# Kernel tuning notes

Hardware: AMD Instinct MI355X
Metric: run time of the kernel (lower is better)

The kernel has to match this reference:

```python
import jax, jax.numpy as jnp
import numpy as np

EPS = 1e-9
LN_EPS = 1e-5

def _ln(t, g, b):
    m = t.mean(-1, keepdims=True)
    v = ((t - m) ** 2).mean(-1, keepdims=True)
    return (t - m) / jnp.sqrt(v + LN_EPS) * g + b

def _dwconv(t, w, b):
    # t: (B,S,H), w: (H,1,4) depthwise. torch pads 3 on both sides then slices [:S],
    # which equals causal left-pad of 3.
    y = jax.lax.conv_general_dilated(
        t.transpose(0, 2, 1), w, window_strides=(1,), padding=[(3, 0)],
        feature_group_count=w.shape[0], dimension_numbers=("NCH", "OIH", "NCH"))
    return y.transpose(0, 2, 1) + b

def _forward(x, Wq, Wk, Wv, Wo, Wg, We1, We2, Wd1, Wd2, Wa1, Wa2,
             conv_w, conv_b, qn_g, qn_b, kn_g, kn_b, mW1, mb1, mW2, mb2, chunk_size):
    B, S, D = x.shape
    H = Wk.shape[1]
    M = mW1.shape[0]
    q = x @ Wq; k = x @ Wk; v = x @ Wv
    eta = jax.nn.softplus((x @ We1) @ We2)
    delta = jax.nn.softplus((x @ Wd1) @ Wd2)
    alpha = jax.nn.sigmoid((x @ Wa1) @ Wa2)
    q = _ln(_dwconv(q, conv_w, conv_b), qn_g, qn_b)  # computed but unused downstream, as in source
    k = _ln(_dwconv(k, conv_w, conv_b), kn_g, kn_b)
    v = _dwconv(v, conv_w, conv_b)
    n = S // chunk_size
    chunk = lambda t: t.reshape(B, n, chunk_size, H).transpose(1, 0, 2, 3)  # (n,B,C,H)
    xs = (chunk(k), chunk(v), chunk(eta), chunk(delta), chunk(alpha))
    state0 = (jnp.broadcast_to(mW1, (B, M, H)), jnp.broadcast_to(mb1, (B, M)),
              jnp.broadcast_to(mW2, (B, H, M)), jnp.broadcast_to(mb2, (B, H)))

    def step(state, inp):
        W1, b1, W2, b2 = state
        kc, vc, ec, dc, ac = inp  # each (B,C,H)
        inter = jnp.einsum("bch,bmh->bcm", kc, W1) + b1[:, None, :]
        act = jax.nn.gelu(inter, approximate=False)
        out = jnp.einsum("bcm,bhm->bch", act, W2) + b2[:, None, :]
        err = out - vc
        en = jnp.sqrt(jnp.sum(err * err, axis=-1, keepdims=True))  # (B,C,1)
        grad = jnp.where(en > dc, dc * err / (en + EPS), err)
        aw = ac[:, -1, :].mean(-1)[:, None, None]
        ew = ec[:, -1, :].mean(-1)[:, None, None]
        us = grad.mean(1, keepdims=True)   # (B,1,H)
        am = act.mean(1, keepdims=True)    # (B,1,M)
        W1g = jnp.einsum("bom,boh->bmh", am, us)
        W2g = jnp.einsum("boh,bom->bhm", us, am)
        nW1 = aw * W1 - ew * W1g
        nW2 = aw * W2 - ew * W2g
        ab = ac[:, -1, :]; eb = ec[:, -1, :]
        b2u = grad.mean(1)
        b1u = jnp.einsum("bch,bhm->bcm", grad, nW2).mean(1)
        nb2 = ab * b2 - eb * b2u
        nb1 = ab.mean(-1, keepdims=True) * b1 - eb.mean(-1, keepdims=True) * b1u
        # torch updates state under no_grad -> detach
        new_state = jax.tree_util.tree_map(jax.lax.stop_gradient, (nW1, nb1, nW2, nb2))
        return new_state, out

    _, outs = jax.lax.scan(step, state0, xs)  # (n,B,C,H)
    combined = outs.transpose(1, 0, 2, 3).reshape(B, S, H)
    return (combined @ Wo) * jax.nn.sigmoid(x @ Wg)

def setup_inputs():
    key = jax.random.key(0)
    B, S, D, H, M, R = 4, 4096, 1024, 128, 256, 64
    ks = jax.random.split(key, 23)
    g = lambda i, shp, s: jax.random.normal(ks[i], shp, jnp.float32) * s
    return {
        "x": g(0, (B, S, D), 1.0),
        "Wq": g(1, (D, H), 0.02), "Wk": g(2, (D, H), 0.02), "Wv": g(3, (D, H), 0.02),
        "Wo": g(4, (H, D), 0.02), "Wg": g(5, (D, D), 0.02),
        "We1": g(6, (D, R), 0.02), "We2": g(7, (R, H), 0.02),
        "Wd1": g(8, (D, R), 0.02), "Wd2": g(9, (R, H), 0.02),
        "Wa1": g(10, (D, R), 0.02), "Wa2": g(11, (R, H), 0.02),
        "conv_w": g(12, (H, 1, 4), 0.2), "conv_b": g(13, (H,), 0.02),
        "qn_g": jnp.ones((H,), jnp.float32), "qn_b": jnp.zeros((H,), jnp.float32),
        "kn_g": jnp.ones((H,), jnp.float32), "kn_b": jnp.zeros((H,), jnp.float32),
        "mW1": g(14, (M, H), 0.05), "mb1": g(15, (M,), 0.02),
        "mW2": g(16, (H, M), 0.05), "mb2": g(17, (H,), 0.02),
        "chunk_size": 64,
    }

def reference(x, Wq, Wk, Wv, Wo, Wg, We1, We2, Wd1, Wd2, Wa1, Wa2,
              conv_w, conv_b, qn_g, qn_b, kn_g, kn_b, mW1, mb1, mW2, mb2, chunk_size):
    return _forward(x, Wq, Wk, Wv, Wo, Wg, We1, We2, Wd1, Wd2, Wa1, Wa2,
                    conv_w, conv_b, qn_g, qn_b, kn_g, kn_b, mW1, mb1, mW2, mb2, chunk_size)
```

## Files before the change

kernel.cpp:

```cpp
#include <hip/hip_runtime.h>
#include <math.h>

#define Bq 4
#define Sq 4096
#define Dq 1024
#define Hq 128
#define Mq 256
#define Rq 64
#define Cq 64
#define NCHUNK 64
#define BSq (Bq*Sq)

typedef __attribute__((ext_vector_type(8))) short short8;
typedef __attribute__((ext_vector_type(4))) float f32x4;

__device__ __forceinline__ float softplusf_(float x){
  return fmaxf(x,0.f) + log1pf(expf(-fabsf(x)));
}
__device__ __forceinline__ float sigmoidf_(float x){
  return 1.f/(1.f+__expf(-x));
}
__device__ __forceinline__ unsigned short bf16rn(float x){
  unsigned u = __float_as_uint(x);
  u += 0x7fffu + ((u>>16)&1u);
  return (unsigned short)(u>>16);
}
__device__ __forceinline__ float bf16tof(unsigned short s){
  return __uint_as_float(((unsigned)s)<<16);
}
__device__ __forceinline__ unsigned cvt_pk_bf16(float a, float b){
  unsigned r;
  asm("v_cvt_pk_bf16_f32 %0, %1, %2" : "=v"(r) : "v"(a), "v"(b));
  return r;
}
__device__ __forceinline__ float lo16f(unsigned p){ return __uint_as_float(p<<16); }
__device__ __forceinline__ float hi16f(unsigned p){ return __uint_as_float(p & 0xffff0000u); }
union pk8 { unsigned u[4]; short8 s; };

__device__ __forceinline__ float gelu_fast(float x){
  float z  = x*0.70710678118f;
  float az = fabsf(z);
  float t  = __builtin_amdgcn_rcpf(fmaf(0.3275911f, az, 1.f));
  float p  = fmaf(t, 1.061405429f, -1.453152027f);
  p = fmaf(t, p, 1.421413741f);
  p = fmaf(t, p, -0.284496736f);
  p = fmaf(t, p, 0.254829592f);
  p = p*t;
  float e  = __expf(-az*az);
  float er = copysignf(1.f - p*e, z);
  return 0.5f*x*(1.f + er);
}

template<int BN, int ACT>
__global__ __launch_bounds__(256) void gemm_bf3(
    const float* __restrict__ Af,
    const unsigned short* __restrict__ BhT, const unsigned short* __restrict__ BlT,
    float* __restrict__ C, const float* __restrict__ gate, int N, int K)
{
  constexpr int BM = 128;
  constexpr int PK = 40;
  constexpr int TN = BN/32;
  __shared__ __align__(16) unsigned short As[2][BM*PK];
  __shared__ __align__(16) unsigned short Bs[2][BN*PK];
  const int tid = threadIdx.x;
  const int bm = blockIdx.y*BM, bn = blockIdx.x*BN;
  const int wv = tid>>6, lane = tid&63;
  const int n16 = lane&15, q = lane>>4;
  const int wm = wv>>1, wn = wv&1;

  f32x4 acc[4][TN];
  #pragma unroll
  for (int i=0;i<4;i++){
    #pragma unroll
    for (int j=0;j<TN;j++){ f32x4 z={0.f,0.f,0.f,0.f}; acc[i][j]=z; }
  }
  for (int k0=0;k0<K;k0+=32){
    #pragma unroll
    for (int c0=0;c0<BM*8;c0+=256){
      int c = c0 + tid;
      int row = c>>3, kg = (c&7)*4;
      float4 v = *(const float4*)&Af[(size_t)(bm+row)*K + k0+kg];
      unsigned hp0 = cvt_pk_bf16(v.x, v.y), hp1 = cvt_pk_bf16(v.z, v.w);
      unsigned lp0 = cvt_pk_bf16(v.x-lo16f(hp0), v.y-hi16f(hp0));
      unsigned lp1 = cvt_pk_bf16(v.z-lo16f(hp1), v.w-hi16f(hp1));
      int off = row*PK+kg;
      *(unsigned*)&As[0][off]   = hp0;
      *(unsigned*)&As[0][off+2] = hp1;
      *(unsigned*)&As[1][off]   = lp0;
      *(unsigned*)&As[1][off+2] = lp1;
    }
    #pragma unroll
    for (int c0=0;c0<BN*4;c0+=256){
      int c = c0 + tid;
      int row = c>>2, kg = (c&3)*8;
      *(short8*)&Bs[0][row*PK+kg] = *(const short8*)&BhT[(size_t)(bn+row)*K + k0+kg];
      *(short8*)&Bs[1][row*PK+kg] = *(const short8*)&BlT[(size_t)(bn+row)*K + k0+kg];
    }
    __syncthreads();
    short8 a_h[4], a_l[4], b_h[TN], b_l[TN];
    #pragma unroll
    for (int i=0;i<4;i++){
      int r = wm*64 + i*16 + n16;
      a_h[i] = *(const short8*)&As[0][r*PK + q*8];
      a_l[i] = *(const short8*)&As[1][r*PK + q*8];
    }
    #pragma unroll
    for (int j=0;j<TN;j++){
      int r = wn*(BN/2) + j*16 + n16;
      b_h[j] = *(const short8*)&Bs[0][r*PK + q*8];
      b_l[j] = *(const short8*)&Bs[1][r*PK + q*8];
    }
    #pragma unroll
    for (int i=0;i<4;i++){
      #pragma unroll
      for (int j=0;j<TN;j++){
        acc[i][j] = __builtin_amdgcn_mfma_f32_16x16x32_bf16(a_h[i], b_h[j], acc[i][j], 0,0,0);
        acc[i][j] = __builtin_amdgcn_mfma_f32_16x16x32_bf16(a_l[i], b_h[j], acc[i][j], 0,0,0);
        acc[i][j] = __builtin_amdgcn_mfma_f32_16x16x32_bf16(a_h[i], b_l[j], acc[i][j], 0,0,0);
      }
    }
    __syncthreads();
  }
  #pragma unroll
  for (int i=0;i<4;i++){
    #pragma unroll
    for (int j=0;j<TN;j++){
      #pragma unroll
      for (int r=0;r<4;r++){
        int row = bm + wm*64 + i*16 + q*4 + r;
        int col = bn + wn*(BN/2) + j*16 + n16;
        float v = acc[i][j][r];
        if (ACT==1) v = softplusf_(v);
        else if (ACT==2) v = sigmoidf_(v);
        else if (ACT==3) v *= sigmoidf_(gate[(size_t)row*N+col]);
        C[(size_t)row*N+col] = v;
      }
    }
  }
}

template<int BN>
__global__ __launch_bounds__(256) void gemm_bb(
    const unsigned short* __restrict__ Ah, const unsigned short* __restrict__ Al,
    const unsigned short* __restrict__ BhT, const unsigned short* __restrict__ BlT,
    float* __restrict__ C0, float* __restrict__ C1, float* __restrict__ C2, int K)
{
  constexpr int BM = 128;
  constexpr int PK = 40;
  constexpr int TN = BN/32;
  __shared__ __align__(16) unsigned short As[2][BM*PK];
  __shared__ __align__(16) unsigned short Bs[2][BN*PK];
  const int tid = threadIdx.x;
  const int bx = blockIdx.x;
  const int bm = blockIdx.y*BM;
  const int bnB = bx*BN;
  float* __restrict__ C = (bx==0) ? C0 : ((bx==1) ? C1 : C2);
  const int wv = tid>>6, lane = tid&63;
  const int n16 = lane&15, q = lane>>4;
  const int wm = wv>>1, wn = wv&1;

  f32x4 acc[4][TN];
  #pragma unroll
  for (int i=0;i<4;i++){
    #pragma unroll
    for (int j=0;j<TN;j++){ f32x4 z={0.f,0.f,0.f,0.f}; acc[i][j]=z; }
  }
  for (int k0=0;k0<K;k0+=32){
    #pragma unroll
    for (int c0=0;c0<BM*4;c0+=256){
      int c = c0 + tid;
      int row = c>>2, kg = (c&3)*8;
      *(short8*)&As[0][row*PK+kg] = *(const short8*)&Ah[(size_t)(bm+row)*K + k0+kg];
      *(short8*)&As[1][row*PK+kg] = *(const short8*)&Al[(size_t)(bm+row)*K + k0+kg];
    }
    #pragma unroll
    for (int c0=0;c0<BN*4;c0+=256){
      int c = c0 + tid;
      int row = c>>2, kg = (c&3)*8;
      *(short8*)&Bs[0][row*PK+kg] = *(const short8*)&BhT[(size_t)(bnB+row)*K + k0+kg];
      *(short8*)&Bs[1][row*PK+kg] = *(const short8*)&BlT[(size_t)(bnB+row)*K + k0+kg];
    }
    __syncthreads();
    short8 a_h[4], a_l[4], b_h[TN], b_l[TN];
    #pragma unroll
    for (int i=0;i<4;i++){
      int r = wm*64 + i*16 + n16;
      a_h[i] = *(const short8*)&As[0][r*PK + q*8];
      a_l[i] = *(const short8*)&As[1][r*PK + q*8];
    }
    #pragma unroll
    for (int j=0;j<TN;j++){
      int r = wn*(BN/2) + j*16 + n16;
      b_h[j] = *(const short8*)&Bs[0][r*PK + q*8];
      b_l[j] = *(const short8*)&Bs[1][r*PK + q*8];
    }
    #pragma unroll
    for (int i=0;i<4;i++){
      #pragma unroll
      for (int j=0;j<TN;j++){
        acc[i][j] = __builtin_amdgcn_mfma_f32_16x16x32_bf16(a_h[i], b_h[j], acc[i][j], 0,0,0);
        acc[i][j] = __builtin_amdgcn_mfma_f32_16x16x32_bf16(a_l[i], b_h[j], acc[i][j], 0,0,0);
        acc[i][j] = __builtin_amdgcn_mfma_f32_16x16x32_bf16(a_h[i], b_l[j], acc[i][j], 0,0,0);
      }
    }
    __syncthreads();
  }
  #pragma unroll
  for (int i=0;i<4;i++){
    #pragma unroll
    for (int j=0;j<TN;j++){
      #pragma unroll
      for (int r=0;r<4;r++){
        int row = bm + wm*64 + i*16 + q*4 + r;
        int col = wn*(BN/2) + j*16 + n16;
        C[(size_t)row*BN+col] = acc[i][j][r];
      }
    }
  }
}

__global__ void splitT(const float* __restrict__ W,
                       unsigned short* __restrict__ hT, unsigned short* __restrict__ lT,
                       int K, int N)
{
  int idx = blockIdx.x*256 + threadIdx.x;
  if (idx >= N*K) return;
  int nn = idx / K, k = idx - nn*K;
  float v = W[(size_t)k*N + nn];
  unsigned short h = bf16rn(v);
  hT[idx] = h;
  lT[idx] = bf16rn(v - bf16tof(h));
}

__global__ __launch_bounds__(256) void splitX(const float* __restrict__ A,
    unsigned short* __restrict__ h, unsigned short* __restrict__ l)
{
  size_t idx = ((size_t)blockIdx.x*256 + threadIdx.x)*4;
  float4 v = *(const float4*)&A[idx];
  unsigned hp0 = cvt_pk_bf16(v.x, v.y), hp1 = cvt_pk_bf16(v.z, v.w);
  unsigned lp0 = cvt_pk_bf16(v.x-lo16f(hp0), v.y-hi16f(hp0));
  unsigned lp1 = cvt_pk_bf16(v.z-lo16f(hp1), v.w-hi16f(hp1));
  *(unsigned*)&h[idx]   = hp0;
  *(unsigned*)&h[idx+2] = hp1;
  *(unsigned*)&l[idx]   = lp0;
  *(unsigned*)&l[idx+2] = lp1;
}

__global__ __launch_bounds__(128) void conv_ln_kernel(
  const float* __restrict__ k_raw, const float* __restrict__ v_raw,
  const float* __restrict__ conv_w, const float* __restrict__ conv_b,
  const float* __restrict__ kn_g, const float* __restrict__ kn_b,
  float* __restrict__ k_out, float* __restrict__ v_out)
{
  int s = blockIdx.x, b = blockIdx.y, which = blockIdx.z;
  int h = threadIdx.x;
  const float* src = (which==0) ? k_raw : v_raw;
  float acc = conv_b[h];
  #pragma unroll
  for (int j=0;j<4;j++){
    int ss = s-3+j;
    if (ss>=0) acc += conv_w[h*4+j]*src[((size_t)b*Sq+ss)*Hq + h];
  }
  if (which==0){
    __shared__ float red[4];
    float sv = acc, s2 = acc*acc;
    #pragma unroll
    for (int off=32; off>0; off>>=1){
      sv += __shfl_down(sv, off, 64);
      s2 += __shfl_down(s2, off, 64);
    }
    if ((h&63)==0){ red[(h>>6)*2]=sv; red[(h>>6)*2+1]=s2; }
    __syncthreads();
    float mean = (red[0]+red[2])*(1.f/128.f);
    float var  = (red[1]+red[3])*(1.f/128.f) - mean*mean;
    float y = (acc-mean)*rsqrtf(var+1e-5f)*kn_g[h]+kn_b[h];
    k_out[((size_t)b*Sq+s)*Hq + h] = y;
  } else {
    v_out[((size_t)b*Sq+s)*Hq + h] = acc;
  }
}

#define OFF_KCH   0
#define OFF_KCL   16384
#define OFF_ACTH  32768
#define OFF_SAM   65536
#define OFF_SUS   66560
#define OFF_PEN   67072
#define OFF_DRED  70144
#define OFF_SUU   78336
#define OFF_SAB   78368
#define OFF_SEB   78880
#define OFF_SABP  79392
#define OFF_SEBP  79400
#define LDS_TOTAL 79408

__global__ __launch_bounds__(512, 2) void fused_scan_wg(
  const float* __restrict__ k_ln, const float* __restrict__ v_c,
  const float* __restrict__ eta, const float* __restrict__ delta,
  const float* __restrict__ alpha,
  const float* __restrict__ mW1, const float* __restrict__ mb1,
  const float* __restrict__ mW2, const float* __restrict__ mb2,
  float* __restrict__ combined,
  const float* __restrict__ x,
  const unsigned short* __restrict__ WgTh, const unsigned short* __restrict__ WgTl,
  float* __restrict__ glog)
{
  __shared__ __align__(16) char smem[LDS_TOTAL];
  const int blk = blockIdx.x;
  const int tid = threadIdx.x;
  const int wv = tid >> 6;
  const int lane = tid & 63;
  const int n = lane & 15;
  const int q = lane >> 4;

  if (blk >= 4){
    unsigned short* As_h = (unsigned short*)smem;
    unsigned short* As_l = As_h + 128*40;
    unsigned short* Bs_h = As_l + 128*40;
    unsigned short* Bs_l = Bs_h + 128*40;
    const int g = blk - 4;
    const int bm = (g>>3)*128, bn = (g&7)*128;
    const int wm = wv&3, wn = wv>>2;
    f32x4 acc[2][4];
    #pragma unroll
    for (int i=0;i<2;i++){
      #pragma unroll
      for (int j=0;j<4;j++){ f32x4 z={0.f,0.f,0.f,0.f}; acc[i][j]=z; }
    }
    for (int k0=0;k0<Dq;k0+=32){
      #pragma unroll
      for (int r=0;r<2;r++){
        int idx = tid + 512*r;
        int row = idx>>3, kg = (idx&7)*4;
        float4 v = *(const float4*)&x[(size_t)(bm+row)*Dq + k0+kg];
        unsigned hp0 = cvt_pk_bf16(v.x, v.y), hp1 = cvt_pk_bf16(v.z, v.w);
        unsigned lp0 = cvt_pk_bf16(v.x-lo16f(hp0), v.y-hi16f(hp0));
        unsigned lp1 = cvt_pk_bf16(v.z-lo16f(hp1), v.w-hi16f(hp1));
        int off = row*40+kg;
        *(unsigned*)&As_h[off]   = hp0;
        *(unsigned*)&As_h[off+2] = hp1;
        *(unsigned*)&As_l[off]   = lp0;
        *(unsigned*)&As_l[off+2] = lp1;
      }
      {
        int row = tid>>2, kg = (tid&3)*8;
        *(short8*)&Bs_h[row*40+kg] = *(const short8*)&WgTh[(size_t)(bn+row)*Dq + k0+kg];
        *(short8*)&Bs_l[row*40+kg] = *(const short8*)&WgTl[(size_t)(bn+row)*Dq + k0+kg];
      }
      __syncthreads();
      short8 a_h[2], a_l[2], b_h[4], b_l[4];
      #pragma unroll
      for (int i=0;i<2;i++){
        int r = wm*32 + i*16 + n;
        a_h[i] = *(const short8*)&As_h[r*40 + q*8];
        a_l[i] = *(const short8*)&As_l[r*40 + q*8];
      }
      #pragma unroll
      for (int j=0;j<4;j++){
        int r = wn*64 + j*16 + n;
        b_h[j] = *(const short8*)&Bs_h[r*40 + q*8];
        b_l[j] = *(const short8*)&Bs_l[r*40 + q*8];
      }
      #pragma unroll
      for (int i=0;i<2;i++){
        #pragma unroll
        for (int j=0;j<4;j++){
          acc[i][j] = __builtin_amdgcn_mfma_f32_16x16x32_bf16(a_h[i], b_h[j], acc[i][j], 0,0,0);
          acc[i][j] = __builtin_amdgcn_mfma_f32_16x16x32_bf16(a_l[i], b_h[j], acc[i][j], 0,0,0);
          acc[i][j] = __builtin_amdgcn_mfma_f32_16x16x32_bf16(a_h[i], b_l[j], acc[i][j], 0,0,0);
        }
      }
      __syncthreads();
    }
    #pragma unroll
    for (int i=0;i<2;i++){
      #pragma unroll
      for (int j=0;j<4;j++){
        #pragma unroll
        for (int r=0;r<4;r++){
          int row = bm + wm*32 + i*16 + q*4 + r;
          int col = bn + wn*64 + j*16 + n;
          glog[(size_t)row*Dq+col] = acc[i][j][r];
        }
      }
    }
    return;
  }

  unsigned short* kc_hi  = (unsigned short*)(smem + OFF_KCH);
  unsigned short* kc_lo  = (unsigned short*)(smem + OFF_KCL);
  unsigned short* act_hi = (unsigned short*)(smem + OFF_ACTH);
  float* Sam = (float*)(smem + OFF_SAM);
  float* Sus = (float*)(smem + OFF_SUS);
  float* pen = (float*)(smem + OFF_PEN);
  float* Dred= (float*)(smem + OFF_DRED);
  float* Suu = (float*)(smem + OFF_SUU);
  float* Sab = (float*)(smem + OFF_SAB);
  float* Seb = (float*)(smem + OFF_SEB);
  float* Sabp = (float*)(smem + OFF_SABP);
  float* Sebp = (float*)(smem + OFF_SEBP);

  const int b = blk;
  const int h = wv*16 + n;
  float w1m[2][4][8];
  float w2m[8][8];
  float b1reg[2];
  float b2n[4];
  #pragma unroll
  for (int tt=0;tt<2;tt++){
    int m = (2*wv+tt)*16 + n;
    #pragma unroll
    for (int ks=0;ks<4;ks++){
      const float* p = mW1 + (size_t)m*Hq + ks*32 + q*8;
      #pragma unroll
      for (int j=0;j<8;j++) w1m[tt][ks][j] = p[j];
    }
    b1reg[tt] = mb1[m];
  }
  {
    #pragma unroll
    for (int ks2=0;ks2<8;ks2++){
      const float* p = mW2 + (size_t)h*Mq + ks2*32 + q*8;
      #pragma unroll
      for (int j=0;j<8;j++) w2m[ks2][j] = p[j];
    }
    #pragma unroll
    for (int r=0;r<4;r++) b2n[r] = mb2[wv*16 + q*4 + r];
  }
  float aw = 0.f, ew = 0.f;
  float am_own[2] = {0.f, 0.f};

  float4 pf[4];
  {
    const size_t base0 = (size_t)b*Sq*Hq;
    #pragma unroll
    for (int r4=0;r4<4;r4++){
      int i4 = tid + 512*r4;
      pf[r4] = *(const float4*)(k_ln + base0 + (size_t)i4*4);
    }
  }

  for (int t=0; t<NCHUNK; ++t){
    const size_t base = ((size_t)b*Sq + (size_t)t*Cq)*Hq;
    #pragma unroll
    for (int r4=0;r4<4;r4++){
      int i4 = tid + 512*r4;
      int c = i4>>5, h0 = (i4&31)<<2;
      float4 v = pf[r4];
      int pg  = (h0>>3) ^ (c & 15);
      int off = c*Hq + (pg<<3) + (h0&7);
      unsigned hp0 = cvt_pk_bf16(v.x, v.y), hp1 = cvt_pk_bf16(v.z, v.w);
      unsigned lp0 = cvt_pk_bf16(v.x-lo16f(hp0), v.y-hi16f(hp0));
      unsigned lp1 = cvt_pk_bf16(v.z-lo16f(hp1), v.w-hi16f(hp1));
      *(unsigned*)&kc_hi[off]   = hp0;
      *(unsigned*)&kc_hi[off+2] = hp1;
      *(unsigned*)&kc_lo[off]   = lp0;
      *(unsigned*)&kc_lo[off+2] = lp1;
    }
    float ab_=0.f, eb_=0.f;
    if (tid < 128){
      ab_ = alpha[base + 63*Hq + tid];
      eb_ = eta[base + 63*Hq + tid];
    }
    __syncthreads();

    if (t > 0){
      float4 s0[4], s1[4];
      #pragma unroll
      for (int ks=0;ks<4;ks++){
        s0[ks] = *(const float4*)&Sus[ks*32 + q*8];
        s1[ks] = *(const float4*)&Sus[ks*32 + q*8 + 4];
      }
      float4 u0 = *(const float4*)&Suu[0];
      float4 u1 = *(const float4*)&Suu[4];
      float uu = u0.x+u0.y+u0.z+u0.w+u1.x+u1.y+u1.z+u1.w;
      #pragma unroll
      for (int tt=0;tt<2;tt++){
        int m = (2*wv+tt)*16 + n;
        float amm = am_own[tt];
        float eam = ew*amm;
        #pragma unroll
        for (int ks=0;ks<4;ks++){
          #pragma unroll
          for (int j=0;j<4;j++){
            w1m[tt][ks][j]   = aw*w1m[tt][ks][j]   - eam*s0[ks][j];
            w1m[tt][ks][j+4] = aw*w1m[tt][ks][j+4] - eam*s1[ks][j];
          }
        }
        float dsum = 0.f;
        #pragma unroll
        for (int w8=0;w8<8;w8++) dsum += Dred[w8*256 + m];
        b1reg[tt] = aw*b1reg[tt] - ew*(aw*dsum - ew*uu*amm);
      }
    }

    f32x4 acc1[2][4];
    #pragma unroll
    for (int tt=0;tt<2;tt++){
      #pragma unroll
      for (int ct=0;ct<4;ct++){ f32x4 z={0.f,0.f,0.f,0.f}; acc1[tt][ct]=z; }
    }
    __builtin_amdgcn_s_setprio(1);
    #pragma unroll
    for (int ks=0;ks<4;ks++){
      pk8 BH[2], BL[2];
      #pragma unroll
      for (int tt=0;tt<2;tt++){
        #pragma unroll
        for (int jp=0;jp<4;jp++){
          float a0 = w1m[tt][ks][2*jp], a1 = w1m[tt][ks][2*jp+1];
          unsigned hp = cvt_pk_bf16(a0, a1);
          BH[tt].u[jp] = hp;
          BL[tt].u[jp] = cvt_pk_bf16(a0 - lo16f(hp), a1 - hi16f(hp));
        }
      }
      #pragma unroll
      for (int ct=0;ct<4;ct++){
        int c = ct*16 + n;
        int off = c*Hq + ((((ks*4+q)^n))<<3);
        short8 ah = *(const short8*)&kc_hi[off];
        short8 al = *(const short8*)&kc_lo[off];
        #pragma unroll
        for (int tt=0;tt<2;tt++){
          acc1[tt][ct] = __builtin_amdgcn_mfma_f32_16x16x32_bf16(ah, BH[tt].s, acc1[tt][ct], 0,0,0);
          acc1[tt][ct] = __builtin_amdgcn_mfma_f32_16x16x32_bf16(al, BH[tt].s, acc1[tt][ct], 0,0,0);
          acc1[tt][ct] = __builtin_amdgcn_mfma_f32_16x16x32_bf16(ah, BL[tt].s, acc1[tt][ct], 0,0,0);
        }
      }
    }
    __builtin_amdgcn_s_setprio(0);
    #pragma unroll
    for (int tt=0;tt<2;tt++){
      int m = (2*wv+tt)*16 + n;
      float b1v = b1reg[tt];
      float amsum = 0.f;
      #pragma unroll
      for (int ct=0;ct<4;ct++){
        #pragma unroll
        for (int r=0;r<4;r++){
          float g = gelu_fast(acc1[tt][ct][r] + b1v);
          amsum += g;
          int c = ct*16 + q*4 + r;
          int pg = (m>>3) ^ (c & 15);
          act_hi[c*Mq + (pg<<3) + (m&7)] = bf16rn(g);
        }
      }
      amsum += __shfl_xor(amsum, 16, 64);
      amsum += __shfl_xor(amsum, 32, 64);
      am_own[tt] = amsum*(1.f/64.f);
      if (q==0) Sam[m] = am_own[tt];
    }
    if (tid < 128){ Sab[tid] = ab_; Seb[tid] = eb_; }
    if (wv < 2){
      float a2 = ab_, e2 = eb_;
      #pragma unroll
      for (int mk=1;mk<64;mk<<=1){ a2 += __shfl_xor(a2,mk,64); e2 += __shfl_xor(e2,mk,64); }
      if (lane==0){ Sabp[wv] = a2; Sebp[wv] = e2; }
    }
    __syncthreads();

    float vv[4][4], dd[4][4];
    #pragma unroll
    for (int ct=0;ct<4;ct++){
      #pragma unroll
      for (int r=0;r<4;r++){
        int c = ct*16 + n;
        int h2 = wv*16 + q*4 + r;
        vv[ct][r] = v_c[base + (size_t)c*Hq + h2];
        dd[ct][r] = delta[base + (size_t)c*Hq + h2];
      }
    }

    f32x4 acc2[4];
    #pragma unroll
    for (int ct=0;ct<4;ct++){ f32x4 z={0.f,0.f,0.f,0.f}; acc2[ct]=z; }
    __builtin_amdgcn_s_setprio(1);
    #pragma unroll
    for (int ks2=0;ks2<8;ks2++){
      pk8 BH, BL;
      #pragma unroll
      for (int jp=0;jp<4;jp++){
        float a0 = w2m[ks2][2*jp], a1 = w2m[ks2][2*jp+1];
        unsigned hp = cvt_pk_bf16(a0, a1);
        BH.u[jp] = hp;
        BL.u[jp] = cvt_pk_bf16(a0 - lo16f(hp), a1 - hi16f(hp));
      }
      #pragma unroll
      for (int ct=0;ct<4;ct++){
        int c = ct*16 + n;
        int off = c*Mq + ((((ks2*4+q)^n))<<3);
        short8 ah = *(const short8*)&act_hi[off];
        acc2[ct] = __builtin_amdgcn_mfma_f32_16x16x32_bf16(BH.s, ah, acc2[ct], 0,0,0);
        acc2[ct] = __builtin_amdgcn_mfma_f32_16x16x32_bf16(BL.s, ah, acc2[ct], 0,0,0);
      }
    }
    __builtin_amdgcn_s_setprio(0);

    {
      const size_t basen = ((size_t)b*Sq + (size_t)((t+1<NCHUNK)?(t+1):t)*Cq)*Hq;
      #pragma unroll
      for (int r4=0;r4<4;r4++){
        int i4 = tid + 512*r4;
        pf[r4] = *(const float4*)(k_ln + basen + (size_t)i4*4);
      }
    }

    float err[4][4];
    {
      float* cb = combined + base;
      #pragma unroll
      for (int ct=0;ct<4;ct++){
        #pragma unroll
        for (int r=0;r<4;r++){
          int c = ct*16 + n;
          int h2 = wv*16 + q*4 + r;
          float o = acc2[ct][r] + b2n[r];
          cb[(size_t)c*Hq + h2] = o;
          err[ct][r] = o - vv[ct][r];
        }
      }
      #pragma unroll
      for (int ct=0;ct<4;ct++){
        float s = err[ct][0]*err[ct][0] + err[ct][1]*err[ct][1]
                + err[ct][2]*err[ct][2] + err[ct][3]*err[ct][3];
        s += __shfl_xor(s, 16, 64);
        s += __shfl_xor(s, 32, 64);
        if (q==0) pen[(ct*16+n)*12 + wv] = s;
      }
    }
    __syncthreads();

    aw = (Sabp[0]+Sabp[1])*(1.f/128.f);
    ew = (Sebp[0]+Sebp[1])*(1.f/128.f);

    float en_c[4];
    #pragma unroll
    for (int ct=0;ct<4;ct++){
      int c = ct*16 + n;
      float4 e0 = *(const float4*)&pen[c*12];
      float4 e1 = *(const float4*)&pen[c*12+4];
      en_c[ct] = sqrtf(e0.x+e0.y+e0.z+e0.w+e1.x+e1.y+e1.z+e1.w);
    }
    float us_r[4];
    #pragma unroll
    for (int r=0;r<4;r++){
      float s = 0.f;
      #pragma unroll
      for (int ct=0;ct<4;ct++){
        float e = err[ct][r];
        float dvv = dd[ct][r];
        float en = en_c[ct];
        float g = (en > dvv) ? dvv*e*__builtin_amdgcn_rcpf(en+1e-9f) : e;
        s += g;
      }
      s += __shfl_xor(s,1,64); s += __shfl_xor(s,2,64);
      s += __shfl_xor(s,4,64); s += __shfl_xor(s,8,64);
      us_r[r] = s*(1.f/64.f);
    }
    if (n==0){
      #pragma unroll
      for (int r=0;r<4;r++) Sus[wv*16 + q*4 + r] = us_r[r];
    }
    {
      float uun = us_r[0]*us_r[0] + us_r[1]*us_r[1]
                + us_r[2]*us_r[2] + us_r[3]*us_r[3];
      uun += __shfl_xor(uun, 16, 64);
      uun += __shfl_xor(uun, 32, 64);
      if (lane==0) Suu[wv] = uun;
    }
    #pragma unroll
    for (int r=0;r<4;r++){
      int h2 = wv*16 + q*4 + r;
      b2n[r] = Sab[h2]*b2n[r] - Seb[h2]*us_r[r];
    }
    float ush;
    {
      int src = (n>>2)<<4;
      float p0 = __shfl(us_r[0], src, 64);
      float p1 = __shfl(us_r[1], src, 64);
      float p2 = __shfl(us_r[2], src, 64);
      float p3 = __shfl(us_r[3], src, 64);
      int rr = n&3;
      ush = (rr==0) ? p0 : (rr==1) ? p1 : (rr==2) ? p2 : p3;
    }

    {
      const bool bb0 = (n&1);
      float p1[8][4];
      #pragma unroll
      for (int k2=0;k2<8;k2++){
        #pragma unroll
        for (int l=0;l<4;l++){
          float mine = ush * (bb0 ? w2m[k2][l+4] : w2m[k2][l]);
          float oth  = ush * (bb0 ? w2m[k2][l]   : w2m[k2][l+4]);
          p1[k2][l] = mine + __shfl_xor(oth, 1, 64);
        }
      }
      const bool bb1 = (n>>1)&1;
      float p2[4][4];
      #pragma unroll
      for (int k2=0;k2<4;k2++){
        #pragma unroll
        for (int l=0;l<4;l++){
          float mine = bb1 ? p1[2*k2+1][l] : p1[2*k2][l];
          float oth  = bb1 ? p1[2*k2][l]   : p1[2*k2+1][l];
          p2[k2][l] = mine + __shfl_xor(oth, 2, 64);
        }
      }
      const bool bb2 = (n>>2)&1;
      float p3[2][4];
      #pragma unroll
      for (int k2=0;k2<2;k2++){
        #pragma unroll
        for (int l=0;l<4;l++){
          float mine = bb2 ? p2[2*k2+1][l] : p2[2*k2][l];
          float oth  = bb2 ? p2[2*k2][l]   : p2[2*k2+1][l];
          p3[k2][l] = mine + __shfl_xor(oth, 4, 64);
        }
      }
      const bool bb3 = (n>>3)&1;
      float4 p4;
      {
        float m0 = bb3 ? p3[1][0] : p3[0][0];
        float o0 = bb3 ? p3[0][0] : p3[1][0];
        p4.x = m0 + __shfl_xor(o0, 8, 64);
        float m1 = bb3 ? p3[1][1] : p3[0][1];
        float o1 = bb3 ? p3[0][1] : p3[1][1];
        p4.y = m1 + __shfl_xor(o1, 8, 64);
        float m2 = bb3 ? p3[1][2] : p3[0][2];
        float o2 = bb3 ? p3[0][2] : p3[1][2];
        p4.z = m2 + __shfl_xor(o2, 8, 64);
        float m3 = bb3 ? p3[1][3] : p3[0][3];
        float o3 = bb3 ? p3[0][3] : p3[1][3];
        p4.w = m3 + __shfl_xor(o3, 8, 64);
      }
      int base_m = (n>>1)*32 + q*8 + (n&1)*4;
      *(float4*)&Dred[wv*256 + base_m] = p4;
    }

    {
      float eus = ew*ush;
      #pragma unroll
      for (int ks2=0;ks2<8;ks2++){
        float4 a0 = *(const float4*)&Sam[ks2*32 + q*8];
        float4 a1 = *(const float4*)&Sam[ks2*32 + q*8 + 4];
        #pragma unroll
        for (int j=0;j<4;j++){
          w2m[ks2][j]   = aw*w2m[ks2][j]   - eus*a0[j];
          w2m[ks2][j+4] = aw*w2m[ks2][j+4] - eus*a1[j];
        }
      }
    }
  }
}

extern "C" void kernel_launch(void* const* d_in, const int* in_sizes, int n_in,
                              void* d_out, int out_size, void* d_ws, size_t ws_size,
                              hipStream_t stream)
{
  const float* x    = (const float*)d_in[0];
  const float* Wk   = (const float*)d_in[2];
  const float* Wv   = (const float*)d_in[3];
  const float* Wo   = (const float*)d_in[4];
  const float* Wg   = (const float*)d_in[5];
  const float* We1  = (const float*)d_in[6];
  const float* We2  = (const float*)d_in[7];
  const float* Wd1  = (const float*)d_in[8];
  const float* Wd2  = (const float*)d_in[9];
  const float* Wa1  = (const float*)d_in[10];
  const float* Wa2  = (const float*)d_in[11];
  const float* conv_w = (const float*)d_in[12];
  const float* conv_b = (const float*)d_in[13];
  const float* kn_g = (const float*)d_in[16];
  const float* kn_b = (const float*)d_in[17];
  const float* mW1  = (const float*)d_in[18];
  const float* mb1  = (const float*)d_in[19];
  const float* mW2  = (const float*)d_in[20];
  const float* mb2  = (const float*)d_in[21];
  float* out = (float*)d_out;

  float* ws = (float*)d_ws;
  size_t o = 0;
  float* k_raw = ws + o; o += (size_t)BSq*Hq;
  float* v_raw = ws + o; o += (size_t)BSq*Hq;
  float* te    = ws + o; o += (size_t)BSq*Rq;
  float* td    = ws + o; o += (size_t)BSq*Rq;
  float* ta    = ws + o; o += (size_t)BSq*Rq;
  float* glog  = ws + o; o += (size_t)BSq*Dq;
  float* etab  = ws + o; o += (size_t)BSq*Hq;
  float* deltab= ws + o; o += (size_t)BSq*Hq;
  float* alphab= ws + o; o += (size_t)BSq*Hq;
  float* k_ln  = ws + o; o += (size_t)BSq*Hq;
  float* v_c   = ws + o; o += (size_t)BSq*Hq;
  float* comb  = ws + o; o += (size_t)BSq*Hq;
  unsigned short* us = (unsigned short*)(ws + o);
  size_t u = 0;
  unsigned short *WkvTh = us+u; u += (size_t)2*Hq*Dq;
  unsigned short *WkvTl = us+u; u += (size_t)2*Hq*Dq;
  unsigned short *WedaTh= us+u; u += (size_t)3*Rq*Dq;
  unsigned short *WedaTl= us+u; u += (size_t)3*Rq*Dq;
  unsigned short *WgTh = us+u; u += (size_t)Dq*Dq;  unsigned short *WgTl = us+u; u += (size_t)Dq*Dq;
  unsigned short *We2Th= us+u; u += (size_t)Hq*Rq;  unsigned short *We2Tl= us+u; u += (size_t)Hq*Rq;
  unsigned short *Wd2Th= us+u; u += (size_t)Hq*Rq;  unsigned short *Wd2Tl= us+u; u += (size_t)Hq*Rq;
  unsigned short *Wa2Th= us+u; u += (size_t)Hq*Rq;  unsigned short *Wa2Tl= us+u; u += (size_t)Hq*Rq;
  unsigned short *WoTh = us+u; u += (size_t)Dq*Hq;  unsigned short *WoTl = us+u; u += (size_t)Dq*Hq;

  unsigned short* xh = (unsigned short*)glog;
  unsigned short* xl = xh + (size_t)BSq*Dq;

  splitT<<<(Hq*Dq+255)/256, 256, 0, stream>>>(Wk,  WkvTh,          WkvTl,          Dq, Hq);
  splitT<<<(Hq*Dq+255)/256, 256, 0, stream>>>(Wv,  WkvTh+(size_t)Hq*Dq, WkvTl+(size_t)Hq*Dq, Dq, Hq);
  splitT<<<(Rq*Dq+255)/256, 256, 0, stream>>>(We1, WedaTh,          WedaTl,          Dq, Rq);
  splitT<<<(Rq*Dq+255)/256, 256, 0, stream>>>(Wd1, WedaTh+(size_t)Rq*Dq, WedaTl+(size_t)Rq*Dq, Dq, Rq);
  splitT<<<(Rq*Dq+255)/256, 256, 0, stream>>>(Wa1, WedaTh+(size_t)2*Rq*Dq, WedaTl+(size_t)2*Rq*Dq, Dq, Rq);
  splitT<<<(Dq*Dq+255)/256, 256, 0, stream>>>(Wg,  WgTh,  WgTl,  Dq, Dq);
  splitT<<<(Hq*Rq+255)/256, 256, 0, stream>>>(We2, We2Th, We2Tl, Rq, Hq);
  splitT<<<(Hq*Rq+255)/256, 256, 0, stream>>>(Wd2, Wd2Th, Wd2Tl, Rq, Hq);
  splitT<<<(Hq*Rq+255)/256, 256, 0, stream>>>(Wa2, Wa2Th, Wa2Tl, Rq, Hq);
  splitT<<<(Dq*Hq+255)/256, 256, 0, stream>>>(Wo,  WoTh,  WoTl,  Hq, Dq);
  splitX<<<(size_t)BSq*Dq/4/256, 256, 0, stream>>>(x, xh, xl);

  dim3 blk(256);
  gemm_bb<128><<<dim3(2, BSq/128), blk, 0, stream>>>(xh, xl, WkvTh, WkvTl, k_raw, v_raw, nullptr, Dq);
  gemm_bb<64> <<<dim3(3, BSq/128), blk, 0, stream>>>(xh, xl, WedaTh, WedaTl, te, td, ta, Dq);
  gemm_bf3<128,1><<<dim3(1, BSq/128), blk, 0, stream>>>(te, We2Th, We2Tl, etab,   nullptr, Hq, Rq);
  gemm_bf3<128,1><<<dim3(1, BSq/128), blk, 0, stream>>>(td, Wd2Th, Wd2Tl, deltab, nullptr, Hq, Rq);
  gemm_bf3<128,2><<<dim3(1, BSq/128), blk, 0, stream>>>(ta, Wa2Th, Wa2Tl, alphab, nullptr, Hq, Rq);
  conv_ln_kernel<<<dim3(Sq, Bq, 2), dim3(128), 0, stream>>>(
      k_raw, v_raw, conv_w, conv_b, kn_g, kn_b, k_ln, v_c);
  fused_scan_wg<<<dim3(4 + (BSq/128)*(Dq/128)), dim3(512), 0, stream>>>(
      k_ln, v_c, etab, deltab, alphab, mW1, mb1, mW2, mb2, comb,
      x, WgTh, WgTl, glog);
  gemm_bf3<128,3><<<dim3(Dq/128, BSq/128), blk, 0, stream>>>(comb, WoTh, WoTl, out, glog, Dq, Hq);
}
```

Measured before the change: 1.436 ms.

## Merge weight-split and eda second-stage launches, vectorize scan loads and stores

Replaces ten splitT launches with one splitT_all kernel that walks every weight segment, and merges the three eta/delta/alpha second-stage GEMMs into one gemm_eda2 launch selected by blockIdx.x. In the scan kernel, the v_c and delta loads move to the top of each chunk as float4 vector loads, and the combined output and Sab/Seb reads become float4 accesses. Paired 32-bit LDS stores are also packed into 64-bit stores. The aim is to cut launch overhead and memory instruction count, at the cost of more live registers in the scan loop.

```diff
diff --git a/kernel.cpp b/kernel.cpp
--- a/kernel.cpp
+++ b/kernel.cpp
@@ -13,6 +13,23 @@
 
 typedef __attribute__((ext_vector_type(8))) short short8;
 typedef __attribute__((ext_vector_type(4))) float f32x4;
+typedef __attribute__((ext_vector_type(2))) unsigned int uintx2;
+
+#define U_WKVTH  ((size_t)0)
+#define U_WKVTL  (U_WKVTH + (size_t)2*Hq*Dq)
+#define U_WEDATH (U_WKVTL + (size_t)2*Hq*Dq)
+#define U_WEDATL (U_WEDATH + (size_t)3*Rq*Dq)
+#define U_WGTH   (U_WEDATL + (size_t)3*Rq*Dq)
+#define U_WGTL   (U_WGTH + (size_t)Dq*Dq)
+#define U_WE2TH  (U_WGTL + (size_t)Dq*Dq)
+#define U_WE2TL  (U_WE2TH + (size_t)Hq*Rq)
+#define U_WD2TH  (U_WE2TL + (size_t)Hq*Rq)
+#define U_WD2TL  (U_WD2TH + (size_t)Hq*Rq)
+#define U_WA2TH  (U_WD2TL + (size_t)Hq*Rq)
+#define U_WA2TL  (U_WA2TH + (size_t)Hq*Rq)
+#define U_WOTH   (U_WA2TL + (size_t)Hq*Rq)
+#define U_WOTL   (U_WOTH + (size_t)Dq*Hq)
+#define U_END    (U_WOTL + (size_t)Dq*Hq)
 
 __device__ __forceinline__ float softplusf_(float x){
   return fmaxf(x,0.f) + log1pf(expf(-fabsf(x)));
@@ -84,10 +101,9 @@
       unsigned lp0 = cvt_pk_bf16(v.x-lo16f(hp0), v.y-hi16f(hp0));
       unsigned lp1 = cvt_pk_bf16(v.z-lo16f(hp1), v.w-hi16f(hp1));
       int off = row*PK+kg;
-      *(unsigned*)&As[0][off]   = hp0;
-      *(unsigned*)&As[0][off+2] = hp1;
-      *(unsigned*)&As[1][off]   = lp0;
-      *(unsigned*)&As[1][off+2] = lp1;
+      uintx2 th = {hp0, hp1}, tl = {lp0, lp1};
+      *(uintx2*)&As[0][off] = th;
+      *(uintx2*)&As[1][off] = tl;
     }
     #pragma unroll
     for (int c0=0;c0<BN*4;c0+=256){
@@ -219,17 +235,122 @@
   }
 }
 
-__global__ void splitT(const float* __restrict__ W,
-                       unsigned short* __restrict__ hT, unsigned short* __restrict__ lT,
-                       int K, int N)
+__global__ __launch_bounds__(256) void gemm_eda2(
+    const float* __restrict__ te, const float* __restrict__ td, const float* __restrict__ ta,
+    const unsigned short* __restrict__ usb,
+    float* __restrict__ etab, float* __restrict__ deltab, float* __restrict__ alphab)
 {
-  int idx = blockIdx.x*256 + threadIdx.x;
-  if (idx >= N*K) return;
-  int nn = idx / K, k = idx - nn*K;
-  float v = W[(size_t)k*N + nn];
-  unsigned short h = bf16rn(v);
-  hT[idx] = h;
-  lT[idx] = bf16rn(v - bf16tof(h));
+  constexpr int BM = 128, PK = 40, BN = 128, TN = 4, K = Rq, N = Hq;
+  __shared__ __align__(16) unsigned short As[2][BM*PK];
+  __shared__ __align__(16) unsigned short Bs[2][BN*PK];
+  const int tid = threadIdx.x;
+  const int bx = blockIdx.x;
+  const int bm = blockIdx.y*BM;
+  const float* __restrict__ Af = (bx==0) ? te : (bx==1) ? td : ta;
+  const unsigned short* __restrict__ BhT = usb + ((bx==0) ? U_WE2TH : (bx==1) ? U_WD2TH : U_WA2TH);
+  const unsigned short* __restrict__ BlT = usb + ((bx==0) ? U_WE2TL : (bx==1) ? U_WD2TL : U_WA2TL);
+  float* __restrict__ C = (bx==0) ? etab : (bx==1) ? deltab : alphab;
+  const int wv = tid>>6, lane = tid&63;
+  const int n16 = lane&15, q = lane>>4;
+  const int wm = wv>>1, wn = wv&1;
+
+  f32x4 acc[4][TN];
+  #pragma unroll
+  for (int i=0;i<4;i++){
+    #pragma unroll
+    for (int j=0;j<TN;j++){ f32x4 z={0.f,0.f,0.f,0.f}; acc[i][j]=z; }
+  }
+  for (int k0=0;k0<K;k0+=32){
+    #pragma unroll
+    for (int c0=0;c0<BM*8;c0+=256){
+      int c = c0 + tid;
+      int row = c>>3, kg = (c&7)*4;
+      float4 v = *(const float4*)&Af[(size_t)(bm+row)*K + k0+kg];
+      unsigned hp0 = cvt_pk_bf16(v.x, v.y), hp1 = cvt_pk_bf16(v.z, v.w);
+      unsigned lp0 = cvt_pk_bf16(v.x-lo16f(hp0), v.y-hi16f(hp0));
+      unsigned lp1 = cvt_pk_bf16(v.z-lo16f(hp1), v.w-hi16f(hp1));
+      int off = row*PK+kg;
+      uintx2 th = {hp0, hp1}, tl = {lp0, lp1};
+      *(uintx2*)&As[0][off] = th;
+      *(uintx2*)&As[1][off] = tl;
+    }
+    #pragma unroll
+    for (int c0=0;c0<BN*4;c0+=256){
+      int c = c0 + tid;
+      int row = c>>2, kg = (c&3)*8;
+      *(short8*)&Bs[0][row*PK+kg] = *(const short8*)&BhT[(size_t)row*K + k0+kg];
+      *(short8*)&Bs[1][row*PK+kg] = *(const short8*)&BlT[(size_t)row*K + k0+kg];
+    }
+    __syncthreads();
+    short8 a_h[4], a_l[4], b_h[TN], b_l[TN];
+    #pragma unroll
+    for (int i=0;i<4;i++){
+      int r = wm*64 + i*16 + n16;
+      a_h[i] = *(const short8*)&As[0][r*PK + q*8];
+      a_l[i] = *(const short8*)&As[1][r*PK + q*8];
+    }
+    #pragma unroll
+    for (int j=0;j<TN;j++){
+      int r = wn*(BN/2) + j*16 + n16;
+      b_h[j] = *(const short8*)&Bs[0][r*PK + q*8];
+      b_l[j] = *(const short8*)&Bs[1][r*PK + q*8];
+    }
+    #pragma unroll
+    for (int i=0;i<4;i++){
+      #pragma unroll
+      for (int j=0;j<TN;j++){
+        acc[i][j] = __builtin_amdgcn_mfma_f32_16x16x32_bf16(a_h[i], b_h[j], acc[i][j], 0,0,0);
+        acc[i][j] = __builtin_amdgcn_mfma_f32_16x16x32_bf16(a_l[i], b_h[j], acc[i][j], 0,0,0);
+        acc[i][j] = __builtin_amdgcn_mfma_f32_16x16x32_bf16(a_h[i], b_l[j], acc[i][j], 0,0,0);
+      }
+    }
+    __syncthreads();
+  }
+  #pragma unroll
+  for (int i=0;i<4;i++){
+    #pragma unroll
+    for (int j=0;j<TN;j++){
+      #pragma unroll
+      for (int r=0;r<4;r++){
+        int row = bm + wm*64 + i*16 + q*4 + r;
+        int col = wn*(BN/2) + j*16 + n16;
+        float v = acc[i][j][r];
+        v = (bx==2) ? sigmoidf_(v) : softplusf_(v);
+        C[(size_t)row*N+col] = v;
+      }
+    }
+  }
+}
+
+__global__ __launch_bounds__(256) void splitT_all(
+    const float* __restrict__ Wk,  const float* __restrict__ Wv,
+    const float* __restrict__ We1, const float* __restrict__ Wd1,
+    const float* __restrict__ Wa1, const float* __restrict__ Wg,
+    const float* __restrict__ We2, const float* __restrict__ Wd2,
+    const float* __restrict__ Wa2, const float* __restrict__ Wo,
+    unsigned short* __restrict__ usb)
+{
+  size_t idx = (size_t)blockIdx.x*256 + threadIdx.x;
+#define SEG(SRC, DH, DL, K_, N_) \
+  { size_t sz = (size_t)(K_)*(N_); \
+    if (idx < sz){ \
+      int nn = (int)(idx/(K_)); int k = (int)(idx - (size_t)nn*(K_)); \
+      float v = (SRC)[(size_t)k*(N_) + nn]; \
+      unsigned short hh = bf16rn(v); \
+      (DH)[idx] = hh; (DL)[idx] = bf16rn(v - bf16tof(hh)); \
+      return; } \
+    idx -= sz; }
+  SEG(Wk,  usb+U_WKVTH,                    usb+U_WKVTL,                    Dq, Hq)
+  SEG(Wv,  usb+U_WKVTH+(size_t)Hq*Dq,      usb+U_WKVTL+(size_t)Hq*Dq,      Dq, Hq)
+  SEG(We1, usb+U_WEDATH,                   usb+U_WEDATL,                   Dq, Rq)
+  SEG(Wd1, usb+U_WEDATH+(size_t)Rq*Dq,     usb+U_WEDATL+(size_t)Rq*Dq,     Dq, Rq)
+  SEG(Wa1, usb+U_WEDATH+(size_t)2*Rq*Dq,   usb+U_WEDATL+(size_t)2*Rq*Dq,   Dq, Rq)
+  SEG(Wg,  usb+U_WGTH,                     usb+U_WGTL,                     Dq, Dq)
+  SEG(We2, usb+U_WE2TH,                    usb+U_WE2TL,                    Rq, Hq)
+  SEG(Wd2, usb+U_WD2TH,                    usb+U_WD2TL,                    Rq, Hq)
+  SEG(Wa2, usb+U_WA2TH,                    usb+U_WA2TL,                    Rq, Hq)
+  SEG(Wo,  usb+U_WOTH,                     usb+U_WOTL,                     Hq, Dq)
+#undef SEG
 }
 
 __global__ __launch_bounds__(256) void splitX(const float* __restrict__ A,
@@ -240,10 +361,9 @@
   unsigned hp0 = cvt_pk_bf16(v.x, v.y), hp1 = cvt_pk_bf16(v.z, v.w);
   unsigned lp0 = cvt_pk_bf16(v.x-lo16f(hp0), v.y-hi16f(hp0));
   unsigned lp1 = cvt_pk_bf16(v.z-lo16f(hp1), v.w-hi16f(hp1));
-  *(unsigned*)&h[idx]   = hp0;
-  *(unsigned*)&h[idx+2] = hp1;
-  *(unsigned*)&l[idx]   = lp0;
-  *(unsigned*)&l[idx+2] = lp1;
+  uintx2 th = {hp0, hp1}, tl = {lp0, lp1};
+  *(uintx2*)&h[idx] = th;
+  *(uintx2*)&l[idx] = tl;
 }
 
 __global__ __launch_bounds__(128) void conv_ln_kernel(
@@ -337,10 +457,9 @@
         unsigned lp0 = cvt_pk_bf16(v.x-lo16f(hp0), v.y-hi16f(hp0));
         unsigned lp1 = cvt_pk_bf16(v.z-lo16f(hp1), v.w-hi16f(hp1));
         int off = row*40+kg;
-        *(unsigned*)&As_h[off]   = hp0;
-        *(unsigned*)&As_h[off+2] = hp1;
-        *(unsigned*)&As_l[off]   = lp0;
-        *(unsigned*)&As_l[off+2] = lp1;
+        uintx2 th = {hp0, hp1}, tl = {lp0, lp1};
+        *(uintx2*)&As_h[off] = th;
+        *(uintx2*)&As_l[off] = tl;
       }
       {
         int row = tid>>2, kg = (tid&3)*8;
@@ -442,6 +561,13 @@
 
   for (int t=0; t<NCHUNK; ++t){
     const size_t base = ((size_t)b*Sq + (size_t)t*Cq)*Hq;
+    f32x4 vvv[4], ddd[4];
+    #pragma unroll
+    for (int ct=0;ct<4;ct++){
+      size_t off = base + (size_t)(ct*16+n)*Hq + wv*16 + q*4;
+      vvv[ct] = *(const f32x4*)&v_c[off];
+      ddd[ct] = *(const f32x4*)&delta[off];
+    }
     #pragma unroll
     for (int r4=0;r4<4;r4++){
       int i4 = tid + 512*r4;
@@ -452,10 +578,9 @@
       unsigned hp0 = cvt_pk_bf16(v.x, v.y), hp1 = cvt_pk_bf16(v.z, v.w);
       unsigned lp0 = cvt_pk_bf16(v.x-lo16f(hp0), v.y-hi16f(hp0));
       unsigned lp1 = cvt_pk_bf16(v.z-lo16f(hp1), v.w-hi16f(hp1));
-      *(unsigned*)&kc_hi[off]   = hp0;
-      *(unsigned*)&kc_hi[off+2] = hp1;
-      *(unsigned*)&kc_lo[off]   = lp0;
-      *(unsigned*)&kc_lo[off+2] = lp1;
+      uintx2 th = {hp0, hp1}, tl = {lp0, lp1};
+      *(uintx2*)&kc_hi[off] = th;
+      *(uintx2*)&kc_lo[off] = tl;
     }
     float ab_=0.f, eb_=0.f;
     if (tid < 128){
@@ -559,18 +684,6 @@
     }
     __syncthreads();
 
-    float vv[4][4], dd[4][4];
-    #pragma unroll
-    for (int ct=0;ct<4;ct++){
-      #pragma unroll
-      for (int r=0;r<4;r++){
-        int c = ct*16 + n;
-        int h2 = wv*16 + q*4 + r;
-        vv[ct][r] = v_c[base + (size_t)c*Hq + h2];
-        dd[ct][r] = delta[base + (size_t)c*Hq + h2];
-      }
-    }
-
     f32x4 acc2[4];
     #pragma unroll
     for (int ct=0;ct<4;ct++){ f32x4 z={0.f,0.f,0.f,0.f}; acc2[ct]=z; }
@@ -610,14 +723,15 @@
       float* cb = combined + base;
       #pragma unroll
       for (int ct=0;ct<4;ct++){
+        int c = ct*16 + n;
+        f32x4 ov;
         #pragma unroll
         for (int r=0;r<4;r++){
-          int c = ct*16 + n;
-          int h2 = wv*16 + q*4 + r;
           float o = acc2[ct][r] + b2n[r];
-          cb[(size_t)c*Hq + h2] = o;
-          err[ct][r] = o - vv[ct][r];
-        }
+          ov[r] = o;
+          err[ct][r] = o - vvv[ct][r];
+        }
+        *(f32x4*)&cb[(size_t)c*Hq + wv*16 + q*4] = ov;
       }
       #pragma unroll
       for (int ct=0;ct<4;ct++){
@@ -648,7 +762,7 @@
       #pragma unroll
       for (int ct=0;ct<4;ct++){
         float e = err[ct][r];
-        float dvv = dd[ct][r];
+        float dvv = ddd[ct][r];
         float en = en_c[ct];
         float g = (en > dvv) ? dvv*e*__builtin_amdgcn_rcpf(en+1e-9f) : e;
         s += g;
@@ -668,10 +782,11 @@
       uun += __shfl_xor(uun, 32, 64);
       if (lane==0) Suu[wv] = uun;
     }
-    #pragma unroll
-    for (int r=0;r<4;r++){
-      int h2 = wv*16 + q*4 + r;
-      b2n[r] = Sab[h2]*b2n[r] - Seb[h2]*us_r[r];
+    {
+      f32x4 sab = *(const f32x4*)&Sab[wv*16 + q*4];
+      f32x4 seb = *(const f32x4*)&Seb[wv*16 + q*4];
+      #pragma unroll
+      for (int r=0;r<4;r++) b2n[r] = sab[r]*b2n[r] - seb[r]*us_r[r];
     }
     float ush;
     {
@@ -793,43 +908,27 @@
   float* k_ln  = ws + o; o += (size_t)BSq*Hq;
   float* v_c   = ws + o; o += (size_t)BSq*Hq;
   float* comb  = ws + o; o += (size_t)BSq*Hq;
-  unsigned short* us = (unsigned short*)(ws + o);
-  size_t u = 0;
-  unsigned short *WkvTh = us+u; u += (size_t)2*Hq*Dq;
-  unsigned short *WkvTl = us+u; u += (size_t)2*Hq*Dq;
-  unsigned short *WedaTh= us+u; u += (size_t)3*Rq*Dq;
-  unsigned short *WedaTl= us+u; u += (size_t)3*Rq*Dq;
-  unsigned short *WgTh = us+u; u += (size_t)Dq*Dq;  unsigned short *WgTl = us+u; u += (size_t)Dq*Dq;
-  unsigned short *We2Th= us+u; u += (size_t)Hq*Rq;  unsigned short *We2Tl= us+u; u += (size_t)Hq*Rq;
-  unsigned short *Wd2Th= us+u; u += (size_t)Hq*Rq;  unsigned short *Wd2Tl= us+u; u += (size_t)Hq*Rq;
-  unsigned short *Wa2Th= us+u; u += (size_t)Hq*Rq;  unsigned short *Wa2Tl= us+u; u += (size_t)Hq*Rq;
-  unsigned short *WoTh = us+u; u += (size_t)Dq*Hq;  unsigned short *WoTl = us+u; u += (size_t)Dq*Hq;
+  unsigned short* usb = (unsigned short*)(ws + o);
 
   unsigned short* xh = (unsigned short*)glog;
   unsigned short* xl = xh + (size_t)BSq*Dq;
 
-  splitT<<<(Hq*Dq+255)/256, 256, 0, stream>>>(Wk,  WkvTh,          WkvTl,          Dq, Hq);
-  splitT<<<(Hq*Dq+255)/256, 256, 0, stream>>>(Wv,  WkvTh+(size_t)Hq*Dq, WkvTl+(size_t)Hq*Dq, Dq, Hq);
-  splitT<<<(Rq*Dq+255)/256, 256, 0, stream>>>(We1, WedaTh,          WedaTl,          Dq, Rq);
-  splitT<<<(Rq*Dq+255)/256, 256, 0, stream>>>(Wd1, WedaTh+(size_t)Rq*Dq, WedaTl+(size_t)Rq*Dq, Dq, Rq);
-  splitT<<<(Rq*Dq+255)/256, 256, 0, stream>>>(Wa1, WedaTh+(size_t)2*Rq*Dq, WedaTl+(size_t)2*Rq*Dq, Dq, Rq);
-  splitT<<<(Dq*Dq+255)/256, 256, 0, stream>>>(Wg,  WgTh,  WgTl,  Dq, Dq);
-  splitT<<<(Hq*Rq+255)/256, 256, 0, stream>>>(We2, We2Th, We2Tl, Rq, Hq);
-  splitT<<<(Hq*Rq+255)/256, 256, 0, stream>>>(Wd2, Wd2Th, Wd2Tl, Rq, Hq);
-  splitT<<<(Hq*Rq+255)/256, 256, 0, stream>>>(Wa2, Wa2Th, Wa2Tl, Rq, Hq);
-  splitT<<<(Dq*Hq+255)/256, 256, 0, stream>>>(Wo,  WoTh,  WoTl,  Hq, Dq);
+  {
+    size_t total = 2*(size_t)Hq*Dq + 3*(size_t)Rq*Dq + (size_t)Dq*Dq
+                 + 3*(size_t)Hq*Rq + (size_t)Dq*Hq;
+    splitT_all<<<(unsigned)(total/256), 256, 0, stream>>>(
+        Wk, Wv, We1, Wd1, Wa1, Wg, We2, Wd2, Wa2, Wo, usb);
+  }
   splitX<<<(size_t)BSq*Dq/4/256, 256, 0, stream>>>(x, xh, xl);
 
   dim3 blk(256);
-  gemm_bb<128><<<dim3(2, BSq/128), blk, 0, stream>>>(xh, xl, WkvTh, WkvTl, k_raw, v_raw, nullptr, Dq);
-  gemm_bb<64> <<<dim3(3, BSq/128), blk, 0, stream>>>(xh, xl, WedaTh, WedaTl, te, td, ta, Dq);
-  gemm_bf3<128,1><<<dim3(1, BSq/128), blk, 0, stream>>>(te, We2Th, We2Tl, etab,   nullptr, Hq, Rq);
-  gemm_bf3<128,1><<<dim3(1, BSq/128), blk, 0, stream>>>(td, Wd2Th, Wd2Tl, deltab, nullptr, Hq, Rq);
-  gemm_bf3<128,2><<<dim3(1, BSq/128), blk, 0, stream>>>(ta, Wa2Th, Wa2Tl, alphab, nullptr, Hq, Rq);
+  gemm_bb<128><<<dim3(2, BSq/128), blk, 0, stream>>>(xh, xl, usb+U_WKVTH, usb+U_WKVTL, k_raw, v_raw, nullptr, Dq);
+  gemm_bb<64> <<<dim3(3, BSq/128), blk, 0, stream>>>(xh, xl, usb+U_WEDATH, usb+U_WEDATL, te, td, ta, Dq);
+  gemm_eda2<<<dim3(3, BSq/128), blk, 0, stream>>>(te, td, ta, usb, etab, deltab, alphab);
   conv_ln_kernel<<<dim3(Sq, Bq, 2), dim3(128), 0, stream>>>(
       k_raw, v_raw, conv_w, conv_b, kn_g, kn_b, k_ln, v_c);
   fused_scan_wg<<<dim3(4 + (BSq/128)*(Dq/128)), dim3(512), 0, stream>>>(
       k_ln, v_c, etab, deltab, alphab, mW1, mb1, mW2, mb2, comb,
-      x, WgTh, WgTl, glog);
-  gemm_bf3<128,3><<<dim3(Dq/128, BSq/128), blk, 0, stream>>>(comb, WoTh, WoTl, out, glog, Dq, Hq);
-}
+      x, usb+U_WGTH, usb+U_WGTL, glog);
+  gemm_bf3<128,3><<<dim3(Dq/128, BSq/128), blk, 0, stream>>>(comb, usb+U_WOTH, usb+U_WOTL, out, glog, Dq, Hq);
+}
```

Result: faster. 1.307 ms (-9.0%).
